# Kernel tuning notes

Measured on AMD Instinct MI355X. Metric: run time of the kernel, lower is better.

Reference implementation:

```python
import jax, jax.numpy as jnp
import numpy as np

ALPHA = 0.2  # LeakyReLU slope
EPS = 1e-16


def _spgat_layer(x, W, a, row, col, N, concat):
    # h: [N, d]
    h = x @ W
    d = h.shape[1]
    # edge attention: a^T [h_row || h_col]  (pyGAT SpGAT: exp(-leakyrelu(.)))
    f_src = h @ a[:d]   # [N]
    f_dst = h @ a[d:]   # [N]
    e = jnp.exp(-jax.nn.leaky_relu(f_src[row] + f_dst[col], ALPHA))  # [E]
    denom = jax.ops.segment_sum(e, row, num_segments=N) + EPS        # [N]
    num = jax.ops.segment_sum(e[:, None] * h[col], row, num_segments=N)  # [N, d]
    out = num / denom[:, None]
    return jax.nn.elu(out) if concat else out


def _spgat(x, W1, a1, W2, a2, edges):
    row, col = edges[0], edges[1]
    N = x.shape[0]
    h = _spgat_layer(x, W1, a1, row, col, N, concat=True)
    h = _spgat_layer(h, W2, a2, row, col, N, concat=False)
    return jax.nn.elu(h)


def setup_inputs() -> dict:
    key = jax.random.key(0)
    ks = jax.random.split(key, 20)
    VOCAB, NFEAT = 50000, 300
    N_TW, L = 50000, 16
    UV = 50000
    E = 800000
    HID, JOINT, NCLASS = 64, 128, 2
    B = 4096

    inp = {}
    # integer structure (constants)
    inp['features_index'] = jax.random.randint(ks[0], (N_TW, L), 0, VOCAB, dtype=jnp.int32)
    inp['tw_edges'] = jax.random.randint(ks[1], (2, E), 0, N_TW, dtype=jnp.int32)
    inp['ut_edges'] = jax.random.randint(ks[2], (2, E), 0, UV, dtype=jnp.int32)
    inp['tw_graph_idx'] = jax.random.randint(ks[3], (B,), 0, N_TW, dtype=jnp.int32)
    inp['ut_graph_idx'] = jax.random.randint(ks[4], (B,), 0, UV, dtype=jnp.int32)
    # learned parameters
    inp['word_emb'] = jax.random.normal(ks[5], (VOCAB, NFEAT), jnp.float32) * 0.1
    inp['user_emb'] = jax.random.normal(ks[6], (UV, NFEAT), jnp.float32) * 0.1
    def gat_params(k, din, dh, dout):
        k1, k2, k3, k4 = jax.random.split(k, 4)
        return (jax.random.normal(k1, (din, dh), jnp.float32) * (1.0 / np.sqrt(din)),
                jax.random.normal(k2, (2 * dh,), jnp.float32) * 0.1,
                jax.random.normal(k3, (dh, dout), jnp.float32) * (1.0 / np.sqrt(dh)),
                jax.random.normal(k4, (2 * dout,), jnp.float32) * 0.1)
    inp['tw_W1'], inp['tw_a1'], inp['tw_W2'], inp['tw_a2'] = gat_params(ks[7], NFEAT, HID, JOINT)
    inp['tu_W1'], inp['tu_a1'], inp['tu_W2'], inp['tu_a2'] = gat_params(ks[8], NFEAT, HID, JOINT)
    inp['weight_W'] = jax.random.uniform(ks[9], (JOINT, JOINT), jnp.float32, -0.1, 0.1)
    inp['weight_proj'] = jax.random.uniform(ks[10], (JOINT, 1), jnp.float32, -0.1, 0.1)
    inp['out_W'] = jax.random.normal(ks[11], (NCLASS, JOINT), jnp.float32) * (1.0 / np.sqrt(JOINT))
    inp['out_b'] = jnp.zeros((NCLASS,), jnp.float32)
    return inp


def reference(word_emb, user_emb, tw_W1, tw_a1, tw_W2, tw_a2,
              tu_W1, tu_a1, tu_W2, tu_a2, weight_W, weight_proj,
              out_W, out_b, features_index, tw_edges, ut_edges,
              tw_graph_idx, ut_graph_idx):
    # tweet features: mean of word embeddings per tweet  [N_tw, nfeat]
    twt_X = word_emb[features_index].mean(axis=1)
    tw_X = _spgat(twt_X, tw_W1, tw_a1, tw_W2, tw_a2, tw_edges)   # [N_tw, joint]
    tu_X = _spgat(user_emb, tu_W1, tu_a1, tu_W2, tu_a2, ut_edges)  # [uV, joint]
    # attention-weighted fusion of the two views
    u_tw = jnp.tanh(tw_X @ weight_W)
    u_tu = jnp.tanh(tu_X @ weight_W)
    att_tw = jnp.mean(u_tw @ weight_proj, axis=0)  # [1]
    att_tu = jnp.mean(u_tu @ weight_proj, axis=0)  # [1]
    att = jax.nn.softmax(jnp.concatenate([att_tw, att_tu], axis=0))  # [2]
    feat = att[0] * tw_X[tw_graph_idx] + att[1] * tu_X[ut_graph_idx]  # [B, joint]
    logits = feat @ out_W.T + out_b
    return jax.nn.log_softmax(logits, axis=1)
```

## Files before the change

kernel.cpp:

```cpp
#include <hip/hip_runtime.h>
#include <hip/hip_bf16.h>

typedef __hip_bfloat16 bf16;
typedef unsigned int uint32;
typedef __attribute__((ext_vector_type(8))) short s8v;
typedef __attribute__((ext_vector_type(4))) short s4v;
typedef __attribute__((ext_vector_type(8))) short bf8v;
typedef __attribute__((ext_vector_type(4))) float f4v;

#define CAP 64
#define CAPSH 6

__device__ __forceinline__ float waveReduce(float v) {
#pragma unroll
    for (int o = 32; o > 0; o >>= 1) v += __shfl_xor(v, o, 64);
    return v;
}

__device__ __forceinline__ short f2bf(float x) {
    __hip_bfloat16 h = __float2bfloat16(x);
    return *reinterpret_cast<short*>(&h);
}
__device__ __forceinline__ float bf2f(short s) {
    return __uint_as_float(((uint32)(unsigned short)s) << 16);
}
__device__ __forceinline__ uint32 pack2(float x, float y) {
    return (uint32)(unsigned short)f2bf(x) | (((uint32)(unsigned short)f2bf(y)) << 16);
}
__device__ __forceinline__ float blo(uint32 d) { return __uint_as_float(d << 16); }
__device__ __forceinline__ float bhi(uint32 d) { return __uint_as_float(d & 0xffff0000u); }
__device__ __forceinline__ float felu(float x) { return x > 0.f ? x : __expf(x) - 1.f; }

struct WJobs {
    const float* src[5];
    short* dst[5];
    int K[5], N[5], KP[5], total[5];
    int* cursor;
    float* attsum;
    float* vab;
    const float* W2tw; const float* a2tw;
    const float* W2tu; const float* a2tu;
    int N2;
};
__global__ void wtrans_all(WJobs jb) {
    int j = blockIdx.y;
    int i = blockIdx.x * blockDim.x + threadIdx.x;
    if (j == 5) {
        if (i < jb.N2) jb.cursor[i] = i << CAPSH;
        if (i < 2) jb.attsum[i] = 0.f;
        if (i < 256) {
            int br = i >> 7;
            int half = (i >> 6) & 1;
            int k = i & 63;
            const float* W2 = br ? jb.W2tu : jb.W2tw;
            const float* a2 = br ? jb.a2tu : jb.a2tw;
            float s = 0.f;
#pragma unroll 4
            for (int q = 0; q < 128; ++q) s += W2[k * 128 + q] * a2[half * 128 + q];
            jb.vab[i] = s;
        }
        return;
    }
    if (i >= jb.total[j]) return;
    int KP = jb.KP[j];
    int n = i / KP, k = i - n * KP;
    jb.dst[j][i] = f2bf(k < jb.K[j] ? jb.src[j][(size_t)k * jb.N[j] + n] : 0.f);
}

__global__ void scatter8_kernel(const int* __restrict__ rowA, const int* __restrict__ colA,
                                const int* __restrict__ rowB, const int* __restrict__ colB,
                                int* __restrict__ cursor, int* __restrict__ ecol,
                                int E, int NTW, int Wsize) {
    int w = (int)blockIdx.x & 7;
    int i = ((int)blockIdx.x >> 3) * 256 + (int)threadIdx.x;
    int lo = w * Wsize, hi = lo + Wsize;
    int r = -1, c = 0;
    if (i < E) {
        r = rowA[i]; c = colA[i];
    } else if (i < 2 * E) {
        r = NTW + rowB[i - E]; c = colB[i - E];
    }
    if (r >= lo && r < hi) {
        int p0 = atomicAdd(&cursor[r], 1);
        if (p0 < (r << CAPSH) + CAP) ecol[p0] = c;
    }
}

struct GJob {
    const void* A;
    const short* Wt;
    const float* av;
    void* C;
    float* fs;
    float* fd;
    int M;
};

template <typename AT, int K, int KPAD, int N, int CSTORE, bool DO_F, bool DO_ATT>
__global__ __launch_bounds__(256) void mfma_gemm(GJob j0, GJob j1, int nb0,
                                                 float* __restrict__ attsum, int bnd) {
    constexpr int NT = N / 16;
    constexpr int NP = KPAD / 64;
    int t = threadIdx.x;

    __shared__ short As[64 * 72];
    __shared__ short Ws[N * 72];
    __shared__ float red[8];
    int lane = t & 63;
    int wid = t >> 6;
    int col = lane & 15;
    int quad = lane >> 4;

    int bid = blockIdx.x;
    bool sec = bid >= nb0;
    GJob J = sec ? j1 : j0;
    const AT* A = (const AT*)J.A;
    const short* Wt = J.Wt;
    const float* av = J.av;
    int M = J.M;
    int row0 = (sec ? bid - nb0 : bid) * 64;

    f4v acc[NT];
#pragma unroll
    for (int i = 0; i < NT; ++i) { f4v z = {0.f, 0.f, 0.f, 0.f}; acc[i] = z; }

    float4 ra[4];
    s8v rsa[2];
    s8v rb[NT / 2];

    auto issue = [&](int p) {
        int k0 = p * 64;
        if constexpr (sizeof(AT) == 4) {
            const float4* A4 = (const float4*)A;
            int f = t & 15, r0 = t >> 4;
#pragma unroll
            for (int r = 0; r < 4; ++r) {
                int gr = row0 + r0 + 16 * r;
                int f4i = (k0 >> 2) + f;
                float4 v = {0.f, 0.f, 0.f, 0.f};
                if (gr < M && f4i < K / 4) v = A4[(size_t)gr * (K / 4) + f4i];
                ra[r] = v;
            }
        } else {
            int c8 = t & 7, r0 = t >> 3;
#pragma unroll
            for (int r = 0; r < 2; ++r) {
                int gr = row0 + r0 + 32 * r;
                s8v v = {0, 0, 0, 0, 0, 0, 0, 0};
                if (gr < M) v = *(const s8v*)&A[(size_t)gr * K + k0 + c8 * 8];
                rsa[r] = v;
            }
        }
        {
            int c8 = t & 7, r0 = t >> 3;
#pragma unroll
            for (int r = 0; r < NT / 2; ++r)
                rb[r] = *(const s8v*)&Wt[(size_t)(r0 + 32 * r) * KPAD + k0 + c8 * 8];
        }
    };
    auto commit = [&]() {
        if constexpr (sizeof(AT) == 4) {
            int f = t & 15, r0 = t >> 4;
#pragma unroll
            for (int r = 0; r < 4; ++r) {
                float4 v = ra[r];
                s4v sv = {f2bf(v.x), f2bf(v.y), f2bf(v.z), f2bf(v.w)};
                *(s4v*)&As[(r0 + 16 * r) * 72 + f * 4] = sv;
            }
        } else {
            int c8 = t & 7, r0 = t >> 3;
#pragma unroll
            for (int r = 0; r < 2; ++r) *(s8v*)&As[(r0 + 32 * r) * 72 + c8 * 8] = rsa[r];
        }
        int c8 = t & 7, r0 = t >> 3;
#pragma unroll
        for (int r = 0; r < NT / 2; ++r) *(s8v*)&Ws[(r0 + 32 * r) * 72 + c8 * 8] = rb[r];
    };

    issue(0);
    for (int p = 0; p < NP; ++p) {
        __syncthreads();
        commit();
        __syncthreads();
        if (p + 1 < NP) issue(p + 1);
#pragma unroll
        for (int c2 = 0; c2 < 2; ++c2) {
            int ko = c2 * 32 + quad * 8;
            bf8v af = *(const bf8v*)&As[(wid * 16 + col) * 72 + ko];
#pragma unroll
            for (int nt = 0; nt < NT; ++nt) {
                bf8v bf = *(const bf8v*)&Ws[(nt * 16 + col) * 72 + ko];
                acc[nt] = __builtin_amdgcn_mfma_f32_16x16x32_bf16(af, bf, acc[nt], 0, 0, 0);
            }
        }
    }

    int mbase = row0 + wid * 16;
    if constexpr (CSTORE == 1) {
        float* C = (float*)J.C;
#pragma unroll
        for (int nt = 0; nt < NT; ++nt)
#pragma unroll
            for (int r = 0; r < 4; ++r) {
                int gr = mbase + quad * 4 + r;
                if (gr < M) C[(size_t)gr * N + nt * 16 + col] = acc[nt][r];
            }
    } else if constexpr (CSTORE == 2 || CSTORE == 3) {
        short* C = (short*)J.C;
#pragma unroll
        for (int nt = 0; nt < NT; ++nt)
#pragma unroll
            for (int r = 0; r < 4; ++r) {
                int gr = mbase + quad * 4 + r;
                float v = acc[nt][r];
                if constexpr (CSTORE == 3) v = felu(v);
                if (gr < M) C[(size_t)gr * N + nt * 16 + col] = f2bf(v);
            }
    }
    if constexpr (DO_F) {
        if (av) {
            float* fs = J.fs;
            float* fd = J.fd;
            float a0[NT], a1[NT];
#pragma unroll
            for (int nt = 0; nt < NT; ++nt) {
                a0[nt] = av[nt * 16 + col];
                a1[nt] = av[N + nt * 16 + col];
            }
#pragma unroll
            for (int r = 0; r < 4; ++r) {
                float p0 = 0.f, p1 = 0.f;
#pragma unroll
                for (int nt = 0; nt < NT; ++nt) {
                    p0 += acc[nt][r] * a0[nt];
                    p1 += acc[nt][r] * a1[nt];
                }
#pragma unroll
                for (int o = 8; o > 0; o >>= 1) {
                    p0 += __shfl_xor(p0, o, 64);
                    p1 += __shfl_xor(p1, o, 64);
                }
                int gr = mbase + quad * 4 + r;
                if (col == 0 && gr < M) { fs[gr] = p0; fd[gr] = p1; }
            }
        }
    }
    if constexpr (DO_ATT) {
        float s0 = 0.f, s1 = 0.f;
#pragma unroll
        for (int nt = 0; nt < NT; ++nt) {
            float pj = av[nt * 16 + col];
#pragma unroll
            for (int r = 0; r < 4; ++r) {
                int gr = mbase + quad * 4 + r;
                float v = tanhf(acc[nt][r]) * pj;
                if (gr < bnd) s0 += v; else s1 += v;
            }
        }
        s0 = waveReduce(s0);
        s1 = waveReduce(s1);
        if (lane == 0) { red[wid] = s0; red[4 + wid] = s1; }
        __syncthreads();
        if (t == 0) {
            atomicAdd(attsum + 0, red[0] + red[1] + red[2] + red[3]);
            atomicAdd(attsum + 1, red[4] + red[5] + red[6] + red[7]);
        }
    }
}

__global__ void gather_h64(const int* __restrict__ idx, const uint32* __restrict__ P,
                           const float* __restrict__ a,
                           short* __restrict__ H, float* __restrict__ fsv, float* __restrict__ fdv,
                           int N) {
    int wv = (blockIdx.x * blockDim.x + threadIdx.x) >> 6;
    int lane = threadIdx.x & 63;
    if (wv >= N) return;
    int hf = lane >> 5, li = lane & 31;
    const int* ip = idx + wv * 16;
    float a0 = 0.f, a1 = 0.f;
#pragma unroll
    for (int u = 0; u < 8; ++u) {
        int ind = ip[2 * u + hf];
        uint32 d = P[(size_t)ind * 32 + li];
        a0 += blo(d);
        a1 += bhi(d);
    }
    a0 += __shfl_xor(a0, 32, 64);
    a1 += __shfl_xor(a1, 32, 64);
    a0 *= 0.0625f;
    a1 *= 0.0625f;
    if (hf == 0) ((uint32*)H)[(size_t)wv * 32 + li] = pack2(a0, a1);
    float cp = hf ? 0.f : (a0 * a[2 * li] + a1 * a[2 * li + 1]);
    float cq = hf ? 0.f : (a0 * a[64 + 2 * li] + a1 * a[64 + 2 * li + 1]);
    float p = waveReduce(cp);
    float q = waveReduce(cq);
    if (lane == 0) { fsv[wv] = p; fdv[wv] = q; }
}

template <bool ELU, bool F2>
__global__ void agg64t_kernel(const int* __restrict__ cursor, const int* __restrict__ ecol,
                              const float* __restrict__ fs, const float* __restrict__ fd,
                              const uint32* __restrict__ hb, uint32* __restrict__ out,
                              const float* __restrict__ vab,
                              float* __restrict__ fs2, float* __restrict__ fd2,
                              int N2, int NTW) {
    int wv = (blockIdx.x * blockDim.x + threadIdx.x) >> 6;
    int lane = threadIdx.x & 63;
    if (wv >= N2) return;
    int s = wv << CAPSH;
    int ne = min(cursor[wv] - s, CAP);
    int coff = wv < NTW ? 0 : NTW;
    float fsr = fs[wv];
    int cl = 0;
    float el = 0.f;
    if (lane < ne) {
        cl = ecol[s + lane];
        float f = fsr + fd[coff + cl];
        el = __expf(-(f >= 0.f ? f : 0.2f * f));
    }
    int qd = lane >> 4, li = lane & 15;
    const uint2* h2 = (const uint2*)hb;
    float a0 = 0.f, a1 = 0.f, a2 = 0.f, a3 = 0.f, den = 0.f;
    for (int kb = 0; kb < ne; kb += 16) {
        int k0 = kb + qd, k1 = kb + 4 + qd, k2 = kb + 8 + qd, k3 = kb + 12 + qd;
        int c0 = __shfl(cl, k0, 64); float e0 = __shfl(el, k0, 64);
        int c1 = __shfl(cl, k1, 64); float e1 = __shfl(el, k1, 64);
        int c2 = __shfl(cl, k2, 64); float e2 = __shfl(el, k2, 64);
        int c3 = __shfl(cl, k3, 64); float e3 = __shfl(el, k3, 64);
        uint2 d0 = h2[(size_t)(coff + c0) * 16 + li];
        uint2 d1 = h2[(size_t)(coff + c1) * 16 + li];
        uint2 d2 = h2[(size_t)(coff + c2) * 16 + li];
        uint2 d3 = h2[(size_t)(coff + c3) * 16 + li];
        a0 += e0 * blo(d0.x) + e1 * blo(d1.x) + e2 * blo(d2.x) + e3 * blo(d3.x);
        a1 += e0 * bhi(d0.x) + e1 * bhi(d1.x) + e2 * bhi(d2.x) + e3 * bhi(d3.x);
        a2 += e0 * blo(d0.y) + e1 * blo(d1.y) + e2 * blo(d2.y) + e3 * blo(d3.y);
        a3 += e0 * bhi(d0.y) + e1 * bhi(d1.y) + e2 * bhi(d2.y) + e3 * bhi(d3.y);
        den += e0 + e1 + e2 + e3;
    }
    a0 += __shfl_xor(a0, 16, 64); a0 += __shfl_xor(a0, 32, 64);
    a1 += __shfl_xor(a1, 16, 64); a1 += __shfl_xor(a1, 32, 64);
    a2 += __shfl_xor(a2, 16, 64); a2 += __shfl_xor(a2, 32, 64);
    a3 += __shfl_xor(a3, 16, 64); a3 += __shfl_xor(a3, 32, 64);
    den += __shfl_xor(den, 16, 64); den += __shfl_xor(den, 32, 64);
    float inv = 1.f / (den + 1e-16f);
    float v0 = a0 * inv, v1 = a1 * inv, v2 = a2 * inv, v3 = a3 * inv;
    if constexpr (ELU) {
        v0 = felu(v0); v1 = felu(v1); v2 = felu(v2); v3 = felu(v3);
    }
    if (lane < 16) {
        uint2 o = {pack2(v0, v1), pack2(v2, v3)};
        ((uint2*)out)[(size_t)wv * 16 + li] = o;
    }
    if constexpr (F2) {
        const float* vv = vab + (wv < NTW ? 0 : 128);
        float ps = 0.f, pd = 0.f;
        if (lane < 16) {
            ps = v0 * vv[4 * li] + v1 * vv[4 * li + 1] + v2 * vv[4 * li + 2] + v3 * vv[4 * li + 3];
            pd = v0 * vv[64 + 4 * li] + v1 * vv[64 + 4 * li + 1] +
                 v2 * vv[64 + 4 * li + 2] + v3 * vv[64 + 4 * li + 3];
        }
        ps = waveReduce(ps);
        pd = waveReduce(pd);
        if (lane == 0) { fs2[wv] = ps; fd2[wv] = pd; }
    }
}

__global__ void final_kernel(const short* __restrict__ twX, const short* __restrict__ tuX,
                             const int* __restrict__ twi, const int* __restrict__ tui,
                             const float* __restrict__ attsum,
                             const float* __restrict__ outW, const float* __restrict__ outb,
                             float* __restrict__ out, int B, float invNtw, float invNuv) {
    int wave = (blockIdx.x * blockDim.x + threadIdx.x) >> 6;
    int lane = threadIdx.x & 63;
    if (wave >= B) return;
    float z0 = attsum[0] * invNtw, z1 = attsum[1] * invNuv;
    float m = fmaxf(z0, z1);
    float e0 = expf(z0 - m), e1 = expf(z1 - m);
    float a0 = e0 / (e0 + e1), a1 = e1 / (e0 + e1);
    int ti = twi[wave], ui = tui[wave];
    float l0 = 0.f, l1 = 0.f;
#pragma unroll
    for (int p = 0; p < 2; ++p) {
        int j = lane + 64 * p;
        float feat = a0 * bf2f(twX[(size_t)ti * 128 + j]) + a1 * bf2f(tuX[(size_t)ui * 128 + j]);
        l0 += feat * outW[j];
        l1 += feat * outW[128 + j];
    }
    l0 = waveReduce(l0);
    l1 = waveReduce(l1);
    if (lane == 0) {
        l0 += outb[0];
        l1 += outb[1];
        float mm = fmaxf(l0, l1);
        float lse = mm + logf(expf(l0 - mm) + expf(l1 - mm));
        out[wave * 2 + 0] = l0 - lse;
        out[wave * 2 + 1] = l1 - lse;
    }
}

extern "C" void kernel_launch(void* const* d_in, const int* in_sizes, int n_in,
                              void* d_out, int out_size, void* d_ws, size_t ws_size,
                              hipStream_t stream) {
    const int* features_index = (const int*)d_in[0];
    const int* tw_edges = (const int*)d_in[1];
    const int* ut_edges = (const int*)d_in[2];
    const int* tw_gidx = (const int*)d_in[3];
    const int* ut_gidx = (const int*)d_in[4];
    const float* word_emb = (const float*)d_in[5];
    const float* user_emb = (const float*)d_in[6];
    const float* tw_W1 = (const float*)d_in[7];
    const float* tw_a1 = (const float*)d_in[8];
    const float* tw_W2 = (const float*)d_in[9];
    const float* tw_a2 = (const float*)d_in[10];
    const float* tu_W1 = (const float*)d_in[11];
    const float* tu_a1 = (const float*)d_in[12];
    const float* tu_W2 = (const float*)d_in[13];
    const float* tu_a2 = (const float*)d_in[14];
    const float* weight_W = (const float*)d_in[15];
    const float* weight_proj = (const float*)d_in[16];
    const float* out_W = (const float*)d_in[17];
    const float* out_b = (const float*)d_in[18];

    const int E = in_sizes[1] / 2;
    const int NTW = in_sizes[0] / 16;
    const int VOCAB = in_sizes[5] / 300;
    const int UV = in_sizes[6] / 300;
    const int B = in_sizes[3];
    const int N2 = NTW + UV;

    char* ws = (char*)d_ws;
    size_t off = 0;
    auto carve = [&](size_t bytes) -> void* {
        void* p = ws + off;
        off += (bytes + 255) & ~(size_t)255;
        return p;
    };
    float* Pbuf = (float*)carve((size_t)VOCAB * 64 * sizeof(float));
    short* Hb1 = (short*)carve((size_t)N2 * 64 * sizeof(short));
    short* Y = (short*)carve((size_t)N2 * 64 * sizeof(short));
    short* X = (short*)carve((size_t)N2 * 128 * sizeof(short));
    float* f_s = (float*)carve((size_t)N2 * sizeof(float));
    float* f_d = (float*)carve((size_t)N2 * sizeof(float));
    float* f_s2 = (float*)carve((size_t)N2 * sizeof(float));
    float* f_d2 = (float*)carve((size_t)N2 * sizeof(float));
    float* attsum = (float*)carve(256);
    float* vab = (float*)carve(256 * sizeof(float));
    int* cursor = (int*)carve((size_t)N2 * sizeof(int));
    int* ecol = (int*)carve((size_t)N2 * CAP * sizeof(int));
    short* Wt1tw = (short*)carve((size_t)64 * 320 * sizeof(short));
    short* Wt1tu = (short*)carve((size_t)64 * 320 * sizeof(short));
    short* Wt2tw = (short*)carve((size_t)128 * 64 * sizeof(short));
    short* Wt2tu = (short*)carve((size_t)128 * 64 * sizeof(short));
    short* Wta   = (short*)carve((size_t)128 * 128 * sizeof(short));
    short* num1 = ((size_t)VOCAB * 64 * sizeof(float) >= (size_t)N2 * 64 * sizeof(short))
                      ? (short*)Pbuf
                      : (short*)carve((size_t)N2 * 64 * sizeof(short));
    (void)ws_size; (void)n_in; (void)out_size;

    WJobs jb;
    jb.src[0] = tw_W1;    jb.dst[0] = Wt1tw; jb.K[0] = 300; jb.N[0] = 64;  jb.KP[0] = 320; jb.total[0] = 64 * 320;
    jb.src[1] = tu_W1;    jb.dst[1] = Wt1tu; jb.K[1] = 300; jb.N[1] = 64;  jb.KP[1] = 320; jb.total[1] = 64 * 320;
    jb.src[2] = tw_W2;    jb.dst[2] = Wt2tw; jb.K[2] = 64;  jb.N[2] = 128; jb.KP[2] = 64;  jb.total[2] = 128 * 64;
    jb.src[3] = tu_W2;    jb.dst[3] = Wt2tu; jb.K[3] = 64;  jb.N[3] = 128; jb.KP[3] = 64;  jb.total[3] = 128 * 64;
    jb.src[4] = weight_W; jb.dst[4] = Wta;   jb.K[4] = 128; jb.N[4] = 128; jb.KP[4] = 128; jb.total[4] = 128 * 128;
    jb.cursor = cursor;
    jb.attsum = attsum;
    jb.vab = vab;
    jb.W2tw = tw_W2; jb.a2tw = tw_a2;
    jb.W2tu = tu_W2; jb.a2tu = tu_a2;
    jb.N2 = N2;
    {
        int gx = (64 * 320 + 255) / 256;
        int gc = (N2 + 255) / 256;
        if (gc > gx) gx = gc;
        dim3 g(gx, 6);
        wtrans_all<<<g, 256, 0, stream>>>(jb);
    }

    {
        int nchunk = (2 * E + 255) / 256;
        int Wsize = (N2 + 7) / 8;
        scatter8_kernel<<<8 * nchunk, 256, 0, stream>>>(tw_edges, tw_edges + E,
                                                        ut_edges, ut_edges + E,
                                                        cursor, ecol, E, NTW, Wsize);
    }

    {
        GJob a{word_emb, Wt1tw, nullptr, Pbuf, nullptr, nullptr, VOCAB};
        GJob b{user_emb, Wt1tu, tu_a1, Hb1 + (size_t)NTW * 64, f_s + NTW, f_d + NTW, UV};
        int nbw = (VOCAB + 63) / 64, nbu = (UV + 63) / 64;
        mfma_gemm<float, 300, 320, 64, 2, true, false><<<nbw + nbu, 256, 0, stream>>>(
            a, b, nbw, nullptr, 0);
    }
    gather_h64<<<(NTW + 3) / 4, 256, 0, stream>>>(features_index, (const uint32*)Pbuf, tw_a1,
                                                  Hb1, f_s, f_d, NTW);

    agg64t_kernel<true, true><<<(N2 + 3) / 4, 256, 0, stream>>>(
        cursor, ecol, f_s, f_d, (const uint32*)Hb1, (uint32*)num1, vab, f_s2, f_d2, N2, NTW);

    agg64t_kernel<false, false><<<(N2 + 3) / 4, 256, 0, stream>>>(
        cursor, ecol, f_s2, f_d2, (const uint32*)num1, (uint32*)Y, nullptr, nullptr, nullptr,
        N2, NTW);

    {
        int nbtw = (NTW + 63) / 64, nbtu = (UV + 63) / 64;
        GJob a{Y, Wt2tw, nullptr, X, nullptr, nullptr, NTW};
        GJob b{Y + (size_t)NTW * 64, Wt2tu, nullptr, X + (size_t)NTW * 128, nullptr, nullptr, UV};
        mfma_gemm<short, 64, 64, 128, 3, false, false><<<nbtw + nbtu, 256, 0, stream>>>(
            a, b, nbtw, nullptr, 0);
    }

    {
        GJob a{X, Wta, weight_proj, nullptr, nullptr, nullptr, N2};
        int nb = (N2 + 63) / 64;
        mfma_gemm<short, 128, 128, 128, 0, false, true><<<nb, 256, 0, stream>>>(
            a, a, nb, attsum, NTW);
    }

    final_kernel<<<(B + 3) / 4, 256, 0, stream>>>(X, X + (size_t)NTW * 128, tw_gidx, ut_gidx,
                                                  attsum, out_W, out_b, (float*)d_out, B,
                                                  1.0f / (float)NTW, 1.0f / (float)UV);
}
```

Before: 434.3 us.

## Fuse attention projection GEMM into second-layer GEMM epilogue

The view-attention computation (tanh(X@weight_W)@proj summed per view) is now done inside the second-layer GEMM epilogue. ELU'd accumulators are staged to shared memory as bf16 and multiplied by weight_W with MFMA. This removes a separate kernel launch and a full re-read of X from global memory, at the cost of extra shared-memory traffic, syncs and register pressure in that GEMM. Edge loads in the scatter kernel also use nontemporal loads to avoid polluting cache.

```diff
diff --git a/kernel.cpp b/kernel.cpp
--- a/kernel.cpp
+++ b/kernel.cpp
@@ -76,9 +76,11 @@
     int lo = w * Wsize, hi = lo + Wsize;
     int r = -1, c = 0;
     if (i < E) {
-        r = rowA[i]; c = colA[i];
+        r = __builtin_nontemporal_load(rowA + i);
+        c = __builtin_nontemporal_load(colA + i);
     } else if (i < 2 * E) {
-        r = NTW + rowB[i - E]; c = colB[i - E];
+        r = NTW + __builtin_nontemporal_load(rowB + (i - E));
+        c = __builtin_nontemporal_load(colB + (i - E));
     }
     if (r >= lo && r < hi) {
         int p0 = atomicAdd(&cursor[r], 1);
@@ -96,9 +98,10 @@
     int M;
 };
 
-template <typename AT, int K, int KPAD, int N, int CSTORE, bool DO_F, bool DO_ATT>
+template <typename AT, int K, int KPAD, int N, int CSTORE, bool DO_F, bool DO_ATT2>
 __global__ __launch_bounds__(256) void mfma_gemm(GJob j0, GJob j1, int nb0,
-                                                 float* __restrict__ attsum, int bnd) {
+                                                 float* __restrict__ attsum,
+                                                 const short* __restrict__ WtaP) {
     constexpr int NT = N / 16;
     constexpr int NP = KPAD / 64;
     int t = threadIdx.x;
@@ -213,7 +216,7 @@
             for (int r = 0; r < 4; ++r) {
                 int gr = mbase + quad * 4 + r;
                 float v = acc[nt][r];
-                if constexpr (CSTORE == 3) v = felu(v);
+                if constexpr (CSTORE == 3) { v = felu(v); acc[nt][r] = v; }
                 if (gr < M) C[(size_t)gr * N + nt * 16 + col] = f2bf(v);
             }
     }
@@ -245,26 +248,51 @@
             }
         }
     }
-    if constexpr (DO_ATT) {
-        float s0 = 0.f, s1 = 0.f;
+    if constexpr (DO_ATT2) {
+        static_assert(!DO_ATT2 || N == 128, "fused att expects N=128");
+        f4v satt[NT];
+#pragma unroll
+        for (int i = 0; i < NT; ++i) { f4v z = {0.f, 0.f, 0.f, 0.f}; satt[i] = z; }
+#pragma unroll
+        for (int h = 0; h < 2; ++h) {
+            __syncthreads();
+#pragma unroll
+            for (int nt2 = 0; nt2 < 4; ++nt2) {
+#pragma unroll
+                for (int r = 0; r < 4; ++r)
+                    As[(wid * 16 + quad * 4 + r) * 72 + nt2 * 16 + col] =
+                        f2bf(acc[h * 4 + nt2][r]);
+            }
+            {
+                int c8 = t & 7, r0 = t >> 3;
+#pragma unroll
+                for (int r = 0; r < 4; ++r)
+                    *(s8v*)&Ws[(r0 + 32 * r) * 72 + c8 * 8] =
+                        *(const s8v*)&WtaP[(size_t)(r0 + 32 * r) * 128 + h * 64 + c8 * 8];
+            }
+            __syncthreads();
+#pragma unroll
+            for (int c2 = 0; c2 < 2; ++c2) {
+                int ko = c2 * 32 + quad * 8;
+                bf8v af = *(const bf8v*)&As[(wid * 16 + col) * 72 + ko];
+#pragma unroll
+                for (int nt = 0; nt < NT; ++nt) {
+                    bf8v bf = *(const bf8v*)&Ws[(nt * 16 + col) * 72 + ko];
+                    satt[nt] = __builtin_amdgcn_mfma_f32_16x16x32_bf16(af, bf, satt[nt], 0, 0, 0);
+                }
+            }
+        }
+        float s = 0.f;
 #pragma unroll
         for (int nt = 0; nt < NT; ++nt) {
             float pj = av[nt * 16 + col];
 #pragma unroll
-            for (int r = 0; r < 4; ++r) {
-                int gr = mbase + quad * 4 + r;
-                float v = tanhf(acc[nt][r]) * pj;
-                if (gr < bnd) s0 += v; else s1 += v;
-            }
-        }
-        s0 = waveReduce(s0);
-        s1 = waveReduce(s1);
-        if (lane == 0) { red[wid] = s0; red[4 + wid] = s1; }
+            for (int r = 0; r < 4; ++r) s += tanhf(satt[nt][r]) * pj;
+        }
+        s = waveReduce(s);
+        if (lane == 0) red[wid] = s;
         __syncthreads();
-        if (t == 0) {
-            atomicAdd(attsum + 0, red[0] + red[1] + red[2] + red[3]);
-            atomicAdd(attsum + 1, red[4] + red[5] + red[6] + red[7]);
-        }
+        if (t == 0) atomicAdd(attsum + (sec ? 1 : 0), red[0] + red[1] + red[2] + red[3]);
     }
 }
 
@@ -490,7 +518,7 @@
         GJob b{user_emb, Wt1tu, tu_a1, Hb1 + (size_t)NTW * 64, f_s + NTW, f_d + NTW, UV};
         int nbw = (VOCAB + 63) / 64, nbu = (UV + 63) / 64;
         mfma_gemm<float, 300, 320, 64, 2, true, false><<<nbw + nbu, 256, 0, stream>>>(
-            a, b, nbw, nullptr, 0);
+            a, b, nbw, nullptr, nullptr);
     }
     gather_h64<<<(NTW + 3) / 4, 256, 0, stream>>>(features_index, (const uint32*)Pbuf, tw_a1,
                                                   Hb1, f_s, f_d, NTW);
@@ -504,17 +532,11 @@
 
     {
         int nbtw = (NTW + 63) / 64, nbtu = (UV + 63) / 64;
-        GJob a{Y, Wt2tw, nullptr, X, nullptr, nullptr, NTW};
-        GJob b{Y + (size_t)NTW * 64, Wt2tu, nullptr, X + (size_t)NTW * 128, nullptr, nullptr, UV};
-        mfma_gemm<short, 64, 64, 128, 3, false, false><<<nbtw + nbtu, 256, 0, stream>>>(
-            a, b, nbtw, nullptr, 0);
-    }
-
-    {
-        GJob a{X, Wta, weight_proj, nullptr, nullptr, nullptr, N2};
-        int nb = (N2 + 63) / 64;
-        mfma_gemm<short, 128, 128, 128, 0, false, true><<<nb, 256, 0, stream>>>(
-            a, a, nb, attsum, NTW);
+        GJob a{Y, Wt2tw, weight_proj, X, nullptr, nullptr, NTW};
+        GJob b{Y + (size_t)NTW * 64, Wt2tu, weight_proj, X + (size_t)NTW * 128,
+               nullptr, nullptr, UV};
+        mfma_gemm<short, 64, 64, 128, 3, false, true><<<nbtw + nbtu, 256, 0, stream>>>(
+            a, b, nbtw, attsum, Wta);
     }
 
     final_kernel<<<(B + 3) / 4, 256, 0, stream>>>(X, X + (size_t)NTW * 128, tw_gidx, ut_gidx,
```

Result: faster. 415.7 us (-4.3%).
